# Kernel tuning notes

Measured on AMD Instinct MI355X. Metric: run time of the kernel, lower is better.

The kernel has to match this reference:

```python
import jax, jax.numpy as jnp
import numpy as np

N, E = 50000, 640000
FEAT, EMB, HID, B = 128, 128, 512, 32


def setup_inputs() -> dict:
    key = jax.random.key(0)
    ks = jax.random.split(key, 12)
    def w(k, shape, fan_in):
        return jax.random.normal(k, shape, dtype=jnp.float32) / np.sqrt(fan_in)
    return {
        "x": jax.random.normal(ks[0], (N, FEAT), dtype=jnp.float32),
        "edge_index": jax.random.randint(ks[1], (2, E), 0, N, dtype=jnp.int64),
        "last_hidden": jax.random.normal(ks[2], (1, B, HID), dtype=jnp.float32),
        "W1_rel": w(ks[3], (FEAT, EMB), FEAT),
        "W1_root": w(ks[4], (FEAT, EMB), FEAT),
        "b1": jnp.zeros((EMB,), dtype=jnp.float32),
        "W2_rel": w(ks[5], (EMB, EMB), EMB),
        "W2_root": w(ks[6], (EMB, EMB), EMB),
        "b2": jnp.zeros((EMB,), dtype=jnp.float32),
        "Wp": w(ks[7], (HID, EMB), HID),
        "bp": jnp.zeros((EMB,), dtype=jnp.float32),
    }


def _rgcn(h, src, dst, W_rel, W_root, b):
    # transform-then-gather (N < E so cheaper): messages along edges src->dst
    msg = (h @ W_rel)[src]                                   # [E, emb]
    agg = jax.ops.segment_sum(msg, dst, num_segments=N)      # [N, emb]
    deg = jax.ops.segment_sum(jnp.ones((E,), h.dtype), dst, num_segments=N)
    agg = agg / jnp.maximum(deg, 1.0)[:, None]               # mean aggregation (PyG RGCNConv default)
    return agg + h @ W_root + b


def reference(x, edge_index, last_hidden, W1_rel, W1_root, b1, W2_rel, W2_root, b2, Wp, bp):
    src, dst = edge_index[0], edge_index[1]
    h = jax.nn.relu(_rgcn(x, src, dst, W1_rel, W1_root, b1))   # [N, emb]
    h = jax.nn.relu(_rgcn(h, src, dst, W2_rel, W2_root, b2))   # [N, emb]
    message_embed = (last_hidden @ Wp + bp)[0]                 # squeeze(0) -> [B, emb]
    scores = h @ message_embed.T                               # [N, B]
    return jax.nn.log_softmax(scores, axis=0)
```

## Files before the change

kernel.cpp:

```cpp
#include <hip/hip_runtime.h>
#include <hip/hip_bf16.h>

#define N_NODES 50000
#define N_EDGES 640000
#define DUMMY   N_NODES
#define PAD_SSRC 990000

typedef __attribute__((ext_vector_type(8))) short short8;
typedef __attribute__((ext_vector_type(4))) float floatx4;

__device__ __forceinline__ float bf2f(unsigned short u) {
    return __uint_as_float(((unsigned int)u) << 16);
}
__device__ __forceinline__ unsigned short f2bf(float x) {
    unsigned int u = __float_as_uint(x);
    u = (u + 0x7fffu + ((u >> 16) & 1u)) >> 16;
    return (unsigned short)u;
}
__device__ __forceinline__ unsigned char f2f8(float x) {
    int pk = __builtin_amdgcn_cvt_pk_fp8_f32(x, x, 0, false);
    return (unsigned char)(pk & 0xff);
}

__global__ void __launch_bounds__(256) prep_k(const float* __restrict__ W0,
                                              const float* __restrict__ W1,
                                              const float* __restrict__ W2,
                                              const float* __restrict__ W3,
                                              unsigned short* __restrict__ T0,
                                              unsigned short* __restrict__ T1,
                                              unsigned short* __restrict__ T2,
                                              unsigned short* __restrict__ T3,
                                              int* __restrict__ cnt,
                                              const float* __restrict__ lh,
                                              const float* __restrict__ Wp,
                                              const float* __restrict__ bp,
                                              unsigned short* __restrict__ meb,
                                              unsigned short* __restrict__ ssrc,
                                              unsigned char* __restrict__ tbf,
                                              int* __restrict__ total,
                                              const int* __restrict__ dst,
                                              int* __restrict__ rank) {
    int b = blockIdx.x, tid = threadIdx.x;
    bool is_hist;
    int idx;
    if (b < 4414) { is_hist = ((b & 1) == 0); idx = b >> 1; }
    else          { is_hist = true;            idx = 2207 + (b - 4414); }
    if (is_hist) {
        int e = idx * 256 + tid;
        int d = dst[e];
        int r = atomicAdd(&cnt[d], 1);
        rank[e] = (r << 16) | d;
        return;
    }
    int s = idx;
    if (s < 256) {
        int i2 = s * 256 + tid;
        int w = i2 >> 14;
        int r = i2 & 16383;
        int n = r >> 7, k = r & 127;
        const float* W = (w == 0) ? W0 : (w == 1) ? W1 : (w == 2) ? W2 : W3;
        unsigned short* T = (w == 0) ? T0 : (w == 1) ? T1 : (w == 2) ? T2 : T3;
        T[r] = f2bf(W[k * 128 + n]);
    } else if (s < 272) {
        int o = (s - 256) * 256 + tid;
        int i = o >> 7, c = o & 127;
        float acc = bp[c];
        const float4* lr = (const float4*)(lh + i * 512);
        #pragma unroll 4
        for (int k4 = 0; k4 < 128; k4++) {
            float4 v = lr[k4];
            acc += v.x * Wp[(4 * k4 + 0) * 128 + c] + v.y * Wp[(4 * k4 + 1) * 128 + c]
                 + v.z * Wp[(4 * k4 + 2) * 128 + c] + v.w * Wp[(4 * k4 + 3) * 128 + c];
        }
        meb[o] = f2bf(acc);
    } else if (s < 2206) {
        int i = (s - 272) * 256 + tid;
        if (i < PAD_SSRC / 2) ((unsigned int*)ssrc)[i] = 0xC350C350u;
    } else {
        if (tid < 32) ((unsigned int*)(tbf + (size_t)DUMMY * 128))[tid] = 0;
        else if (tid == 32) *total = 0;
    }
}

template <bool AF32>
__device__ __forceinline__ void gemm_dual_body(int bid, int tid,
                                               const void* __restrict__ Ain,
                                               const unsigned short* __restrict__ BtRel,
                                               const unsigned short* __restrict__ BtRoot,
                                               unsigned char* __restrict__ Trel,
                                               unsigned short* __restrict__ Rootb, int M) {
    int wid = tid >> 6, lane = tid & 63;
    int r0 = bid * 32 + (wid >> 1) * 16;
    int ch = (wid & 1) * 64;
    int m = lane & 15, g = lane >> 4;
    int row = r0 + m;
    int rowc = (row < M) ? row : (M - 1);
    short8 a[4];
    if constexpr (AF32) {
        const float* A = (const float*)Ain;
        #pragma unroll
        for (int kt = 0; kt < 4; kt++) {
            const float* p = A + (size_t)rowc * 128 + kt * 32 + g * 8;
            float4 v0 = *(const float4*)p;
            float4 v1 = *(const float4*)(p + 4);
            short8 t;
            t[0] = (short)f2bf(v0.x); t[1] = (short)f2bf(v0.y);
            t[2] = (short)f2bf(v0.z); t[3] = (short)f2bf(v0.w);
            t[4] = (short)f2bf(v1.x); t[5] = (short)f2bf(v1.y);
            t[6] = (short)f2bf(v1.z); t[7] = (short)f2bf(v1.w);
            a[kt] = t;
        }
    } else {
        const unsigned short* A = (const unsigned short*)Ain;
        #pragma unroll
        for (int kt = 0; kt < 4; kt++)
            a[kt] = *(const short8*)(A + (size_t)rowc * 128 + kt * 32 + g * 8);
    }
    floatx4 accR[4], accO[4];
    #pragma unroll
    for (int ct = 0; ct < 4; ct++) {
        accR[ct] = (floatx4)(0.f);
        accO[ct] = (floatx4)(0.f);
    }
    #pragma unroll
    for (int ct = 0; ct < 4; ct++) {
        const unsigned short* br = BtRel  + (size_t)(ch + ct * 16 + m) * 128 + g * 8;
        const unsigned short* bo = BtRoot + (size_t)(ch + ct * 16 + m) * 128 + g * 8;
        short8 bR[4], bO[4];
        #pragma unroll
        for (int kt = 0; kt < 4; kt++) {
            bR[kt] = *(const short8*)(br + kt * 32);
            bO[kt] = *(const short8*)(bo + kt * 32);
        }
        #pragma unroll
        for (int kt = 0; kt < 4; kt++) {
            accR[ct] = __builtin_amdgcn_mfma_f32_16x16x32_bf16(a[kt], bR[kt], accR[ct], 0, 0, 0);
            accO[ct] = __builtin_amdgcn_mfma_f32_16x16x32_bf16(a[kt], bO[kt], accO[ct], 0, 0, 0);
        }
    }
    #pragma unroll
    for (int ct = 0; ct < 4; ct++) {
        #pragma unroll
        for (int rg = 0; rg < 4; rg++) {
            int ro = r0 + g * 4 + rg;
            if (ro < M) {
                int co = ch + ct * 16 + m;
                Trel[(size_t)ro * 128 + co]  = f2f8(accR[ct][rg]);
                Rootb[(size_t)ro * 128 + co] = f2bf(accO[ct][rg]);
            }
        }
    }
}

__global__ void __launch_bounds__(256) allocgemm_k(const int* __restrict__ cnt,
                                                   int* __restrict__ prow,
                                                   int* __restrict__ total,
                                                   const float* __restrict__ A,
                                                   const unsigned short* __restrict__ BtRel,
                                                   const unsigned short* __restrict__ BtRoot,
                                                   unsigned char* __restrict__ Trel,
                                                   unsigned short* __restrict__ Rootb) {
    if (blockIdx.x < 196) {
        __shared__ int sm[256];
        __shared__ int base_s;
        int t = threadIdx.x;
        int i = blockIdx.x * 256 + t;
        int pc = (i < N_NODES) ? ((cnt[i] + 7) & ~7) : 0;
        sm[t] = pc;
        __syncthreads();
        for (int off = 1; off < 256; off <<= 1) {
            int v = (t >= off) ? sm[t - off] : 0;
            __syncthreads();
            sm[t] += v;
            __syncthreads();
        }
        if (t == 255) base_s = atomicAdd(total, sm[255]);
        __syncthreads();
        if (i < N_NODES) prow[i] = base_s + sm[t] - pc;
    } else {
        gemm_dual_body<true>(blockIdx.x - 196, threadIdx.x, A, BtRel, BtRoot, Trel, Rootb, N_NODES);
    }
}

__global__ void __launch_bounds__(256) place_k(const int* __restrict__ src,
                                               const int* __restrict__ prow,
                                               const int* __restrict__ rank,
                                               unsigned short* __restrict__ ssrc) {
    int e = blockIdx.x * 256 + threadIdx.x;
    if (e < N_EDGES) {
        int pk = rank[e];
        int d = pk & 0xffff;
        int r = pk >> 16;
        ssrc[prow[d] + r] = (unsigned short)src[e];
    }
}

__global__ void __launch_bounds__(256) gemm_dual_k(const unsigned short* __restrict__ A,
                                                   const unsigned short* __restrict__ BtRel,
                                                   const unsigned short* __restrict__ BtRoot,
                                                   unsigned char* __restrict__ Trel,
                                                   unsigned short* __restrict__ Rootb, int M) {
    gemm_dual_body<false>(blockIdx.x, threadIdx.x, A, BtRel, BtRoot, Trel, Rootb, M);
}

__global__ void __launch_bounds__(256) agg_k(const int* __restrict__ prow,
                                             const int* __restrict__ cnt,
                                             const unsigned short* __restrict__ ssrc,
                                             const unsigned char* __restrict__ t,
                                             const unsigned short* __restrict__ rootb,
                                             const float* __restrict__ bias,
                                             unsigned short* __restrict__ hout) {
    int node = blockIdx.x * 4 + (threadIdx.x >> 6);
    if (node >= N_NODES) return;
    int lane = threadIdx.x & 63;
    int fl = lane & 31;
    int sh = (lane & 32) >> 1;
    int beg = prow[node];
    int deg = cnt[node];
    int endp = beg + ((deg + 7) & ~7);
    const unsigned char* tf = t + fl * 4;
    float a0=0.f,a1=0.f,a2=0.f,a3=0.f;
    float b0=0.f,b1=0.f,b2=0.f,b3=0.f;
    for (int e = beg; e < endp; e += 16) {
        uint4 w0 = *(const uint4*)(ssrc + e);
        uint4 w1 = (e + 8 < endp) ? *(const uint4*)(ssrc + e + 8)
                                  : make_uint4(0xC350C350u, 0xC350C350u, 0xC350C350u, 0xC350C350u);
        int i0 = (int)((w0.x >> sh) & 0xffffu);
        int i1 = (int)((w0.y >> sh) & 0xffffu);
        int i2 = (int)((w0.z >> sh) & 0xffffu);
        int i3 = (int)((w0.w >> sh) & 0xffffu);
        int i4 = (int)((w1.x >> sh) & 0xffffu);
        int i5 = (int)((w1.y >> sh) & 0xffffu);
        int i6 = (int)((w1.z >> sh) & 0xffffu);
        int i7 = (int)((w1.w >> sh) & 0xffffu);
        unsigned int u0 = *(const unsigned int*)(tf + (size_t)i0 * 128);
        unsigned int u1 = *(const unsigned int*)(tf + (size_t)i1 * 128);
        unsigned int u2 = *(const unsigned int*)(tf + (size_t)i2 * 128);
        unsigned int u3 = *(const unsigned int*)(tf + (size_t)i3 * 128);
        unsigned int u4 = *(const unsigned int*)(tf + (size_t)i4 * 128);
        unsigned int u5 = *(const unsigned int*)(tf + (size_t)i5 * 128);
        unsigned int u6 = *(const unsigned int*)(tf + (size_t)i6 * 128);
        unsigned int u7 = *(const unsigned int*)(tf + (size_t)i7 * 128);
        a0 += __builtin_amdgcn_cvt_f32_fp8(u0, 0) + __builtin_amdgcn_cvt_f32_fp8(u1, 0);
        a1 += __builtin_amdgcn_cvt_f32_fp8(u0, 1) + __builtin_amdgcn_cvt_f32_fp8(u1, 1);
        a2 += __builtin_amdgcn_cvt_f32_fp8(u0, 2) + __builtin_amdgcn_cvt_f32_fp8(u1, 2);
        a3 += __builtin_amdgcn_cvt_f32_fp8(u0, 3) + __builtin_amdgcn_cvt_f32_fp8(u1, 3);
        b0 += __builtin_amdgcn_cvt_f32_fp8(u2, 0) + __builtin_amdgcn_cvt_f32_fp8(u3, 0);
        b1 += __builtin_amdgcn_cvt_f32_fp8(u2, 1) + __builtin_amdgcn_cvt_f32_fp8(u3, 1);
        b2 += __builtin_amdgcn_cvt_f32_fp8(u2, 2) + __builtin_amdgcn_cvt_f32_fp8(u3, 2);
        b3 += __builtin_amdgcn_cvt_f32_fp8(u2, 3) + __builtin_amdgcn_cvt_f32_fp8(u3, 3);
        a0 += __builtin_amdgcn_cvt_f32_fp8(u4, 0) + __builtin_amdgcn_cvt_f32_fp8(u5, 0);
        a1 += __builtin_amdgcn_cvt_f32_fp8(u4, 1) + __builtin_amdgcn_cvt_f32_fp8(u5, 1);
        a2 += __builtin_amdgcn_cvt_f32_fp8(u4, 2) + __builtin_amdgcn_cvt_f32_fp8(u5, 2);
        a3 += __builtin_amdgcn_cvt_f32_fp8(u4, 3) + __builtin_amdgcn_cvt_f32_fp8(u5, 3);
        b0 += __builtin_amdgcn_cvt_f32_fp8(u6, 0) + __builtin_amdgcn_cvt_f32_fp8(u7, 0);
        b1 += __builtin_amdgcn_cvt_f32_fp8(u6, 1) + __builtin_amdgcn_cvt_f32_fp8(u7, 1);
        b2 += __builtin_amdgcn_cvt_f32_fp8(u6, 2) + __builtin_amdgcn_cvt_f32_fp8(u7, 2);
        b3 += __builtin_amdgcn_cvt_f32_fp8(u6, 3) + __builtin_amdgcn_cvt_f32_fp8(u7, 3);
    }
    a0 += b0; a1 += b1; a2 += b2; a3 += b3;
    a0 += __shfl_xor(a0, 32);
    a1 += __shfl_xor(a1, 32);
    a2 += __shfl_xor(a2, 32);
    a3 += __shfl_xor(a3, 32);
    if ((lane & 32) == 0) {
        float inv = 1.f / fmaxf((float)deg, 1.f);
        int f = fl * 4;
        ushort4 r = *(const ushort4*)(rootb + (size_t)node * 128 + f);
        float4 bb = *(const float4*)(bias + f);
        ushort4 o;
        o.x = f2bf(fmaxf(a0 * inv + bf2f(r.x) + bb.x, 0.f));
        o.y = f2bf(fmaxf(a1 * inv + bf2f(r.y) + bb.y, 0.f));
        o.z = f2bf(fmaxf(a2 * inv + bf2f(r.z) + bb.z, 0.f));
        o.w = f2bf(fmaxf(a3 * inv + bf2f(r.w) + bb.w, 0.f));
        *(ushort4*)(hout + (size_t)node * 128 + f) = o;
    }
}

__global__ void __launch_bounds__(256) scores_cs_k(const unsigned short* __restrict__ A,
                                                   const unsigned short* __restrict__ Bt,
                                                   float* __restrict__ S,
                                                   float* __restrict__ pm,
                                                   float* __restrict__ ps) {
    __shared__ float Sl[64][33];
    __shared__ float sm[256], ss[256];
    int tid = threadIdx.x;
    int wid = tid >> 6, lane = tid & 63;
    int r0 = blockIdx.x * 64 + wid * 16;
    int m = lane & 15, g = lane >> 4;
    int row = r0 + m;
    int rowc = (row < N_NODES) ? row : (N_NODES - 1);
    short8 a[4];
    #pragma unroll
    for (int kt = 0; kt < 4; kt++)
        a[kt] = *(const short8*)(A + (size_t)rowc * 128 + kt * 32 + g * 8);
    floatx4 acc[2];
    acc[0] = (floatx4)(0.f);
    acc[1] = (floatx4)(0.f);
    #pragma unroll
    for (int ct = 0; ct < 2; ct++) {
        const unsigned short* b = Bt + (size_t)(ct * 16 + m) * 128 + g * 8;
        #pragma unroll
        for (int kt = 0; kt < 4; kt++) {
            short8 bv = *(const short8*)(b + kt * 32);
            acc[ct] = __builtin_amdgcn_mfma_f32_16x16x32_bf16(a[kt], bv, acc[ct], 0, 0, 0);
        }
    }
    #pragma unroll
    for (int ct = 0; ct < 2; ct++) {
        #pragma unroll
        for (int rg = 0; rg < 4; rg++) {
            int lr = wid * 16 + g * 4 + rg;
            int ro = r0 + g * 4 + rg;
            Sl[lr][ct * 16 + m] = acc[ct][rg];
            if (ro < N_NODES) S[(size_t)ro * 32 + ct * 16 + m] = acc[ct][rg];
        }
    }
    __syncthreads();
    int col = tid & 31, sub = tid >> 5;
    int blkbase = blockIdx.x * 64;
    float mm = -3.4e38f, s = 0.f;
    for (int r = sub; r < 64; r += 8) {
        if (blkbase + r < N_NODES) {
            float v = Sl[r][col];
            if (v > mm) { s = s * __expf(mm - v) + 1.f; mm = v; }
            else        { s += __expf(v - mm); }
        }
    }
    sm[tid] = mm; ss[tid] = s;
    __syncthreads();
    for (int off = 128; off >= 32; off >>= 1) {
        if (tid < off) {
            float m2 = sm[tid + off], s2 = ss[tid + off];
            float M = fmaxf(sm[tid], m2);
            ss[tid] = ss[tid] * __expf(sm[tid] - M) + s2 * __expf(m2 - M);
            sm[tid] = M;
        }
        __syncthreads();
    }
    if (tid < 32) { pm[tid * 782 + blockIdx.x] = sm[tid]; ps[tid * 782 + blockIdx.x] = ss[tid]; }
}

__global__ void __launch_bounds__(256) merge_k(const float* __restrict__ pm,
                                               const float* __restrict__ ps,
                                               float* __restrict__ cmg,
                                               float* __restrict__ clg) {
    __shared__ float sm[256], ss[256];
    int col = blockIdx.x;
    int t = threadIdx.x;
    float m = -3.4e38f, s = 0.f;
    for (int c = t; c < 782; c += 256) {
        float m2 = pm[col * 782 + c], s2 = ps[col * 782 + c];
        float M = fmaxf(m, m2);
        s = s * __expf(m - M) + s2 * __expf(m2 - M);
        m = M;
    }
    sm[t] = m; ss[t] = s;
    __syncthreads();
    for (int off = 128; off > 0; off >>= 1) {
        if (t < off) {
            float m2 = sm[t + off], s2 = ss[t + off];
            float M = fmaxf(sm[t], m2);
            ss[t] = ss[t] * __expf(sm[t] - M) + s2 * __expf(m2 - M);
            sm[t] = M;
        }
        __syncthreads();
    }
    if (t == 0) { cmg[col] = sm[0]; clg[col] = logf(ss[0]); }
}

__global__ void __launch_bounds__(256) final_k(const float* __restrict__ S,
                                               const float* __restrict__ cmg,
                                               const float* __restrict__ clg,
                                               float* __restrict__ out) {
    __shared__ float cc[32];
    int t = threadIdx.x;
    if (t < 32) cc[t] = cmg[t] + clg[t];
    __syncthreads();
    int idx = blockIdx.x * 256 + t;
    if (idx < N_NODES * 32) {
        int b = idx & 31;
        out[idx] = S[idx] - cc[b];
    }
}

extern "C" void kernel_launch(void* const* d_in, const int* in_sizes, int n_in,
                              void* d_out, int out_size, void* d_ws, size_t ws_size,
                              hipStream_t stream) {
    const float* x       = (const float*)d_in[0];
    const int*   ei      = (const int*)d_in[1];
    const float* lh      = (const float*)d_in[2];
    const float* W1_rel  = (const float*)d_in[3];
    const float* W1_root = (const float*)d_in[4];
    const float* b1      = (const float*)d_in[5];
    const float* W2_rel  = (const float*)d_in[6];
    const float* W2_root = (const float*)d_in[7];
    const float* b2      = (const float*)d_in[8];
    const float* Wp      = (const float*)d_in[9];
    const float* bp      = (const float*)d_in[10];
    float* out = (float*)d_out;
    float* ws  = (float*)d_ws;

    unsigned char*  tbf   = (unsigned char*)(ws + 3200000);
    unsigned short* rootb = (unsigned short*)(ws + 4800032);
    unsigned short* hb    = (unsigned short*)(ws + 8000032);
    unsigned short* Wt1r  = (unsigned short*)(ws + 11200032);
    unsigned short* Wt1o  = (unsigned short*)(ws + 11208224);
    unsigned short* Wt2r  = (unsigned short*)(ws + 11216416);
    unsigned short* Wt2o  = (unsigned short*)(ws + 11224608);
    unsigned short* MEb   = (unsigned short*)(ws + 11232800);
    float* pm   = ws + 11234848;
    float* ps   = ws + 11259872;
    float* cmg  = ws + 11284896;
    float* clg  = ws + 11284928;
    int*   cnt  = (int*)(ws + 11284960);
    int*   prow = (int*)(ws + 11334960);
    int*   total= (int*)(ws + 11384961);
    int*   rank = (int*)(ws + 11384964);
    unsigned short* ssrc = (unsigned short*)(ws + 12024964);
    float* S    = ws + 12519964;

    const int* srcp = ei;
    const int* dstp = ei + N_EDGES;

    const int e_grid   = (N_EDGES + 255) / 256;
    const int ew_grid  = (N_NODES * 32 + 255) / 256;
    const int agg_grid = (N_NODES + 3) / 4;
    const int mm_grid  = (N_NODES + 63) / 64;
    const int g32_grid = (N_NODES + 31) / 32;

    hipMemsetAsync(cnt, 0, N_NODES * sizeof(int), stream);

    prep_k<<<4707, 256, 0, stream>>>(W1_rel, W1_root, W2_rel, W2_root,
                                     Wt1r, Wt1o, Wt2r, Wt2o,
                                     cnt, lh, Wp, bp, MEb, ssrc, tbf, total,
                                     dstp, rank);

    allocgemm_k<<<196 + g32_grid, 256, 0, stream>>>(cnt, prow, total,
                                                    x, Wt1r, Wt1o, tbf, rootb);

    place_k<<<e_grid, 256, 0, stream>>>(srcp, prow, rank, ssrc);

    agg_k<<<agg_grid, 256, 0, stream>>>(prow, cnt, ssrc, tbf, rootb, b1, hb);

    gemm_dual_k<<<g32_grid, 256, 0, stream>>>(hb, Wt2r, Wt2o, tbf, rootb, N_NODES);

    agg_k<<<agg_grid, 256, 0, stream>>>(prow, cnt, ssrc, tbf, rootb, b2, hb);

    scores_cs_k<<<mm_grid, 256, 0, stream>>>(hb, MEb, S, pm, ps);

    merge_k<<<32, 256, 0, stream>>>(pm, ps, cmg, clg);

    final_k<<<ew_grid, 256, 0, stream>>>(S, cmg, clg, out);
}
```

Baseline: 259.2 us.

## Privatize degree histogram per XCC to avoid cross-die atomics

```diff
diff --git a/kernel.cpp b/kernel.cpp
--- a/kernel.cpp
+++ b/kernel.cpp
@@ -30,7 +30,7 @@
                                               unsigned short* __restrict__ T1,
                                               unsigned short* __restrict__ T2,
                                               unsigned short* __restrict__ T3,
-                                              int* __restrict__ cnt,
+                                              int* __restrict__ cnt8,
                                               const float* __restrict__ lh,
                                               const float* __restrict__ Wp,
                                               const float* __restrict__ bp,
@@ -48,8 +48,12 @@
     if (is_hist) {
         int e = idx * 256 + tid;
         int d = dst[e];
-        int r = atomicAdd(&cnt[d], 1);
-        rank[e] = (r << 16) | d;
+        int xcc;
+        asm volatile("s_getreg_b32 %0, hwreg(HW_REG_XCC_ID)" : "=s"(xcc));
+        xcc &= 7;
+        int r = __hip_atomic_fetch_add(&cnt8[xcc * N_NODES + d], 1,
+                                       __ATOMIC_RELAXED, __HIP_MEMORY_SCOPE_WORKGROUP);
+        rank[e] = (r << 19) | (xcc << 16) | d;
         return;
     }
     int s = idx;
@@ -152,8 +156,10 @@
     }
 }
 
-__global__ void __launch_bounds__(256) allocgemm_k(const int* __restrict__ cnt,
+__global__ void __launch_bounds__(256) allocgemm_k(const int* __restrict__ cnt8,
+                                                   int* __restrict__ cnt,
                                                    int* __restrict__ prow,
+                                                   int* __restrict__ poff,
                                                    int* __restrict__ total,
                                                    const float* __restrict__ A,
                                                    const unsigned short* __restrict__ BtRel,
@@ -165,7 +171,13 @@
         __shared__ int base_s;
         int t = threadIdx.x;
         int i = blockIdx.x * 256 + t;
-        int pc = (i < N_NODES) ? ((cnt[i] + 7) & ~7) : 0;
+        int deg = 0;
+        int pre[8];
+        if (i < N_NODES) {
+            #pragma unroll
+            for (int c = 0; c < 8; c++) { pre[c] = deg; deg += cnt8[c * N_NODES + i]; }
+        }
+        int pc = (i < N_NODES) ? ((deg + 7) & ~7) : 0;
         sm[t] = pc;
         __syncthreads();
         for (int off = 1; off < 256; off <<= 1) {
@@ -176,22 +188,29 @@
         }
         if (t == 255) base_s = atomicAdd(total, sm[255]);
         __syncthreads();
-        if (i < N_NODES) prow[i] = base_s + sm[t] - pc;
+        if (i < N_NODES) {
+            int base = base_s + sm[t] - pc;
+            prow[i] = base;
+            cnt[i] = deg;
+            #pragma unroll
+            for (int c = 0; c < 8; c++) poff[i * 8 + c] = base + pre[c];
+        }
     } else {
         gemm_dual_body<true>(blockIdx.x - 196, threadIdx.x, A, BtRel, BtRoot, Trel, Rootb, N_NODES);
     }
 }
 
 __global__ void __launch_bounds__(256) place_k(const int* __restrict__ src,
-                                               const int* __restrict__ prow,
+                                               const int* __restrict__ poff,
                                                const int* __restrict__ rank,
                                                unsigned short* __restrict__ ssrc) {
     int e = blockIdx.x * 256 + threadIdx.x;
     if (e < N_EDGES) {
         int pk = rank[e];
         int d = pk & 0xffff;
-        int r = pk >> 16;
-        ssrc[prow[d] + r] = (unsigned short)src[e];
+        int c = (pk >> 16) & 7;
+        int r = (int)(((unsigned)pk) >> 19);
+        ssrc[poff[d * 8 + c] + r] = (unsigned short)src[e];
     }
 }
 
@@ -419,6 +438,8 @@
     int*   rank = (int*)(ws + 11384964);
     unsigned short* ssrc = (unsigned short*)(ws + 12024964);
     float* S    = ws + 12519964;
+    int*   cnt8 = (int*)(ws + 12519964);
+    int*   poff = (int*)(ws + 12519964 + 400000);
 
     const int* srcp = ei;
     const int* dstp = ei + N_EDGES;
@@ -429,17 +450,17 @@
     const int mm_grid  = (N_NODES + 63) / 64;
     const int g32_grid = (N_NODES + 31) / 32;
 
-    hipMemsetAsync(cnt, 0, N_NODES * sizeof(int), stream);
+    hipMemsetAsync(cnt8, 0, 8 * N_NODES * sizeof(int), stream);
 
     prep_k<<<4707, 256, 0, stream>>>(W1_rel, W1_root, W2_rel, W2_root,
                                      Wt1r, Wt1o, Wt2r, Wt2o,
-                                     cnt, lh, Wp, bp, MEb, ssrc, tbf, total,
+                                     cnt8, lh, Wp, bp, MEb, ssrc, tbf, total,
                                      dstp, rank);
 
-    allocgemm_k<<<196 + g32_grid, 256, 0, stream>>>(cnt, prow, total,
+    allocgemm_k<<<196 + g32_grid, 256, 0, stream>>>(cnt8, cnt, prow, poff, total,
                                                     x, Wt1r, Wt1o, tbf, rootb);
 
-    place_k<<<e_grid, 256, 0, stream>>>(srcp, prow, rank, ssrc);
+    place_k<<<e_grid, 256, 0, stream>>>(srcp, poff, rank, ssrc);
 
     agg_k<<<agg_grid, 256, 0, stream>>>(prow, cnt, ssrc, tbf, rootb, b1, hb);
 
```

Measured after the change: 259.7 us. No clear change (+0.2%).

## Fuse neighbor aggregation with following GEMM and scores via LDS-staged tiles

Applied to the files above, without the earlier changes.

```diff
diff --git a/kernel.cpp b/kernel.cpp
--- a/kernel.cpp
+++ b/kernel.cpp
@@ -37,6 +37,7 @@
                                               unsigned short* __restrict__ meb,
                                               unsigned short* __restrict__ ssrc,
                                               unsigned char* __restrict__ tbf,
+                                              unsigned char* __restrict__ tbf2,
                                               int* __restrict__ total,
                                               const int* __restrict__ dst,
                                               int* __restrict__ rank) {
@@ -77,45 +78,21 @@
         int i = (s - 272) * 256 + tid;
         if (i < PAD_SSRC / 2) ((unsigned int*)ssrc)[i] = 0xC350C350u;
     } else {
-        if (tid < 32) ((unsigned int*)(tbf + (size_t)DUMMY * 128))[tid] = 0;
-        else if (tid == 32) *total = 0;
-    }
-}
-
-template <bool AF32>
-__device__ __forceinline__ void gemm_dual_body(int bid, int tid,
-                                               const void* __restrict__ Ain,
-                                               const unsigned short* __restrict__ BtRel,
-                                               const unsigned short* __restrict__ BtRoot,
-                                               unsigned char* __restrict__ Trel,
-                                               unsigned short* __restrict__ Rootb, int M) {
+        if (tid < 32)       ((unsigned int*)(tbf  + (size_t)DUMMY * 128))[tid] = 0;
+        else if (tid < 64)  ((unsigned int*)(tbf2 + (size_t)DUMMY * 128))[tid - 32] = 0;
+        else if (tid == 64) *total = 0;
+    }
+}
+
+__device__ __forceinline__ void gemm_dual_frags(int bid, int tid, const short8 a[4],
+                                                const unsigned short* __restrict__ BtRel,
+                                                const unsigned short* __restrict__ BtRoot,
+                                                unsigned char* __restrict__ Trel,
+                                                unsigned short* __restrict__ Rootb, int M) {
     int wid = tid >> 6, lane = tid & 63;
     int r0 = bid * 32 + (wid >> 1) * 16;
     int ch = (wid & 1) * 64;
     int m = lane & 15, g = lane >> 4;
-    int row = r0 + m;
-    int rowc = (row < M) ? row : (M - 1);
-    short8 a[4];
-    if constexpr (AF32) {
-        const float* A = (const float*)Ain;
-        #pragma unroll
-        for (int kt = 0; kt < 4; kt++) {
-            const float* p = A + (size_t)rowc * 128 + kt * 32 + g * 8;
-            float4 v0 = *(const float4*)p;
-            float4 v1 = *(const float4*)(p + 4);
-            short8 t;
-            t[0] = (short)f2bf(v0.x); t[1] = (short)f2bf(v0.y);
-            t[2] = (short)f2bf(v0.z); t[3] = (short)f2bf(v0.w);
-            t[4] = (short)f2bf(v1.x); t[5] = (short)f2bf(v1.y);
-            t[6] = (short)f2bf(v1.z); t[7] = (short)f2bf(v1.w);
-            a[kt] = t;
-        }
-    } else {
-        const unsigned short* A = (const unsigned short*)Ain;
-        #pragma unroll
-        for (int kt = 0; kt < 4; kt++)
-            a[kt] = *(const short8*)(A + (size_t)rowc * 128 + kt * 32 + g * 8);
-    }
     floatx4 accR[4], accO[4];
     #pragma unroll
     for (int ct = 0; ct < 4; ct++) {
@@ -178,7 +155,26 @@
         __syncthreads();
         if (i < N_NODES) prow[i] = base_s + sm[t] - pc;
     } else {
-        gemm_dual_body<true>(blockIdx.x - 196, threadIdx.x, A, BtRel, BtRoot, Trel, Rootb, N_NODES);
+        int bid = blockIdx.x - 196, tid = threadIdx.x;
+        int wid = tid >> 6, lane = tid & 63;
+        int r0 = bid * 32 + (wid >> 1) * 16;
+        int m = lane & 15, g = lane >> 4;
+        int row = r0 + m;
+        int rowc = (row < N_NODES) ? row : (N_NODES - 1);
+        short8 a[4];
+        #pragma unroll
+        for (int kt = 0; kt < 4; kt++) {
+            const float* p = A + (size_t)rowc * 128 + kt * 32 + g * 8;
+            float4 v0 = *(const float4*)p;
+            float4 v1 = *(const float4*)(p + 4);
+            short8 t8;
+            t8[0] = (short)f2bf(v0.x); t8[1] = (short)f2bf(v0.y);
+            t8[2] = (short)f2bf(v0.z); t8[3] = (short)f2bf(v0.w);
+            t8[4] = (short)f2bf(v1.x); t8[5] = (short)f2bf(v1.y);
+            t8[6] = (short)f2bf(v1.z); t8[7] = (short)f2bf(v1.w);
+            a[kt] = t8;
+        }
+        gemm_dual_frags(bid, tid, a, BtRel, BtRoot, Trel, Rootb, N_NODES);
     }
 }
 
@@ -195,105 +191,166 @@
     }
 }
 
-__global__ void __launch_bounds__(256) gemm_dual_k(const unsigned short* __restrict__ A,
-                                                   const unsigned short* __restrict__ BtRel,
-                                                   const unsigned short* __restrict__ BtRoot,
-                                                   unsigned char* __restrict__ Trel,
-                                                   unsigned short* __restrict__ Rootb, int M) {
-    gemm_dual_body<false>(blockIdx.x, threadIdx.x, A, BtRel, BtRoot, Trel, Rootb, M);
-}
-
-__global__ void __launch_bounds__(256) agg_k(const int* __restrict__ prow,
-                                             const int* __restrict__ cnt,
-                                             const unsigned short* __restrict__ ssrc,
-                                             const unsigned char* __restrict__ t,
-                                             const unsigned short* __restrict__ rootb,
-                                             const float* __restrict__ bias,
-                                             unsigned short* __restrict__ hout) {
-    int node = blockIdx.x * 4 + (threadIdx.x >> 6);
-    if (node >= N_NODES) return;
-    int lane = threadIdx.x & 63;
-    int fl = lane & 31;
-    int sh = (lane & 32) >> 1;
-    int beg = prow[node];
-    int deg = cnt[node];
-    int endp = beg + ((deg + 7) & ~7);
-    const unsigned char* tf = t + fl * 4;
+__device__ __forceinline__ void agg_gather(int node, int sh,
+                                           const int* __restrict__ prow,
+                                           const int* __restrict__ cnt,
+                                           const unsigned short* __restrict__ ssrc,
+                                           const unsigned char* __restrict__ tf,
+                                           float& A0, float& A1, float& A2, float& A3,
+                                           int& DEG) {
     float a0=0.f,a1=0.f,a2=0.f,a3=0.f;
     float b0=0.f,b1=0.f,b2=0.f,b3=0.f;
-    for (int e = beg; e < endp; e += 16) {
-        uint4 w0 = *(const uint4*)(ssrc + e);
-        uint4 w1 = (e + 8 < endp) ? *(const uint4*)(ssrc + e + 8)
-                                  : make_uint4(0xC350C350u, 0xC350C350u, 0xC350C350u, 0xC350C350u);
-        int i0 = (int)((w0.x >> sh) & 0xffffu);
-        int i1 = (int)((w0.y >> sh) & 0xffffu);
-        int i2 = (int)((w0.z >> sh) & 0xffffu);
-        int i3 = (int)((w0.w >> sh) & 0xffffu);
-        int i4 = (int)((w1.x >> sh) & 0xffffu);
-        int i5 = (int)((w1.y >> sh) & 0xffffu);
-        int i6 = (int)((w1.z >> sh) & 0xffffu);
-        int i7 = (int)((w1.w >> sh) & 0xffffu);
-        unsigned int u0 = *(const unsigned int*)(tf + (size_t)i0 * 128);
-        unsigned int u1 = *(const unsigned int*)(tf + (size_t)i1 * 128);
-        unsigned int u2 = *(const unsigned int*)(tf + (size_t)i2 * 128);
-        unsigned int u3 = *(const unsigned int*)(tf + (size_t)i3 * 128);
-        unsigned int u4 = *(const unsigned int*)(tf + (size_t)i4 * 128);
-        unsigned int u5 = *(const unsigned int*)(tf + (size_t)i5 * 128);
-        unsigned int u6 = *(const unsigned int*)(tf + (size_t)i6 * 128);
-        unsigned int u7 = *(const unsigned int*)(tf + (size_t)i7 * 128);
-        a0 += __builtin_amdgcn_cvt_f32_fp8(u0, 0) + __builtin_amdgcn_cvt_f32_fp8(u1, 0);
-        a1 += __builtin_amdgcn_cvt_f32_fp8(u0, 1) + __builtin_amdgcn_cvt_f32_fp8(u1, 1);
-        a2 += __builtin_amdgcn_cvt_f32_fp8(u0, 2) + __builtin_amdgcn_cvt_f32_fp8(u1, 2);
-        a3 += __builtin_amdgcn_cvt_f32_fp8(u0, 3) + __builtin_amdgcn_cvt_f32_fp8(u1, 3);
-        b0 += __builtin_amdgcn_cvt_f32_fp8(u2, 0) + __builtin_amdgcn_cvt_f32_fp8(u3, 0);
-        b1 += __builtin_amdgcn_cvt_f32_fp8(u2, 1) + __builtin_amdgcn_cvt_f32_fp8(u3, 1);
-        b2 += __builtin_amdgcn_cvt_f32_fp8(u2, 2) + __builtin_amdgcn_cvt_f32_fp8(u3, 2);
-        b3 += __builtin_amdgcn_cvt_f32_fp8(u2, 3) + __builtin_amdgcn_cvt_f32_fp8(u3, 3);
-        a0 += __builtin_amdgcn_cvt_f32_fp8(u4, 0) + __builtin_amdgcn_cvt_f32_fp8(u5, 0);
-        a1 += __builtin_amdgcn_cvt_f32_fp8(u4, 1) + __builtin_amdgcn_cvt_f32_fp8(u5, 1);
-        a2 += __builtin_amdgcn_cvt_f32_fp8(u4, 2) + __builtin_amdgcn_cvt_f32_fp8(u5, 2);
-        a3 += __builtin_amdgcn_cvt_f32_fp8(u4, 3) + __builtin_amdgcn_cvt_f32_fp8(u5, 3);
-        b0 += __builtin_amdgcn_cvt_f32_fp8(u6, 0) + __builtin_amdgcn_cvt_f32_fp8(u7, 0);
-        b1 += __builtin_amdgcn_cvt_f32_fp8(u6, 1) + __builtin_amdgcn_cvt_f32_fp8(u7, 1);
-        b2 += __builtin_amdgcn_cvt_f32_fp8(u6, 2) + __builtin_amdgcn_cvt_f32_fp8(u7, 2);
-        b3 += __builtin_amdgcn_cvt_f32_fp8(u6, 3) + __builtin_amdgcn_cvt_f32_fp8(u7, 3);
+    int deg = 0;
+    if (node < N_NODES) {
+        int beg = prow[node];
+        deg = cnt[node];
+        int endp = beg + ((deg + 7) & ~7);
+        for (int e = beg; e < endp; e += 16) {
+            uint4 w0 = *(const uint4*)(ssrc + e);
+            uint4 w1 = (e + 8 < endp) ? *(const uint4*)(ssrc + e + 8)
+                                      : make_uint4(0xC350C350u, 0xC350C350u, 0xC350C350u, 0xC350C350u);
+            int i0 = (int)((w0.x >> sh) & 0xffffu);
+            int i1 = (int)((w0.y >> sh) & 0xffffu);
+            int i2 = (int)((w0.z >> sh) & 0xffffu);
+            int i3 = (int)((w0.w >> sh) & 0xffffu);
+            int i4 = (int)((w1.x >> sh) & 0xffffu);
+            int i5 = (int)((w1.y >> sh) & 0xffffu);
+            int i6 = (int)((w1.z >> sh) & 0xffffu);
+            int i7 = (int)((w1.w >> sh) & 0xffffu);
+            unsigned int u0 = *(const unsigned int*)(tf + (size_t)i0 * 128);
+            unsigned int u1 = *(const unsigned int*)(tf + (size_t)i1 * 128);
+            unsigned int u2 = *(const unsigned int*)(tf + (size_t)i2 * 128);
+            unsigned int u3 = *(const unsigned int*)(tf + (size_t)i3 * 128);
+            unsigned int u4 = *(const unsigned int*)(tf + (size_t)i4 * 128);
+            unsigned int u5 = *(const unsigned int*)(tf + (size_t)i5 * 128);
+            unsigned int u6 = *(const unsigned int*)(tf + (size_t)i6 * 128);
+            unsigned int u7 = *(const unsigned int*)(tf + (size_t)i7 * 128);
+            a0 += __builtin_amdgcn_cvt_f32_fp8(u0, 0) + __builtin_amdgcn_cvt_f32_fp8(u1, 0);
+            a1 += __builtin_amdgcn_cvt_f32_fp8(u0, 1) + __builtin_amdgcn_cvt_f32_fp8(u1, 1);
+            a2 += __builtin_amdgcn_cvt_f32_fp8(u0, 2) + __builtin_amdgcn_cvt_f32_fp8(u1, 2);
+            a3 += __builtin_amdgcn_cvt_f32_fp8(u0, 3) + __builtin_amdgcn_cvt_f32_fp8(u1, 3);
+            b0 += __builtin_amdgcn_cvt_f32_fp8(u2, 0) + __builtin_amdgcn_cvt_f32_fp8(u3, 0);
+            b1 += __builtin_amdgcn_cvt_f32_fp8(u2, 1) + __builtin_amdgcn_cvt_f32_fp8(u3, 1);
+            b2 += __builtin_amdgcn_cvt_f32_fp8(u2, 2) + __builtin_amdgcn_cvt_f32_fp8(u3, 2);
+            b3 += __builtin_amdgcn_cvt_f32_fp8(u2, 3) + __builtin_amdgcn_cvt_f32_fp8(u3, 3);
+            a0 += __builtin_amdgcn_cvt_f32_fp8(u4, 0) + __builtin_amdgcn_cvt_f32_fp8(u5, 0);
+            a1 += __builtin_amdgcn_cvt_f32_fp8(u4, 1) + __builtin_amdgcn_cvt_f32_fp8(u5, 1);
+            a2 += __builtin_amdgcn_cvt_f32_fp8(u4, 2) + __builtin_amdgcn_cvt_f32_fp8(u5, 2);
+            a3 += __builtin_amdgcn_cvt_f32_fp8(u4, 3) + __builtin_amdgcn_cvt_f32_fp8(u5, 3);
+            b0 += __builtin_amdgcn_cvt_f32_fp8(u6, 0) + __builtin_amdgcn_cvt_f32_fp8(u7, 0);
+            b1 += __builtin_amdgcn_cvt_f32_fp8(u6, 1) + __builtin_amdgcn_cvt_f32_fp8(u7, 1);
+            b2 += __builtin_amdgcn_cvt_f32_fp8(u6, 2) + __builtin_amdgcn_cvt_f32_fp8(u7, 2);
+            b3 += __builtin_amdgcn_cvt_f32_fp8(u6, 3) + __builtin_amdgcn_cvt_f32_fp8(u7, 3);
+        }
     }
     a0 += b0; a1 += b1; a2 += b2; a3 += b3;
     a0 += __shfl_xor(a0, 32);
     a1 += __shfl_xor(a1, 32);
     a2 += __shfl_xor(a2, 32);
     a3 += __shfl_xor(a3, 32);
-    if ((lane & 32) == 0) {
-        float inv = 1.f / fmaxf((float)deg, 1.f);
-        int f = fl * 4;
-        ushort4 r = *(const ushort4*)(rootb + (size_t)node * 128 + f);
-        float4 bb = *(const float4*)(bias + f);
-        ushort4 o;
-        o.x = f2bf(fmaxf(a0 * inv + bf2f(r.x) + bb.x, 0.f));
-        o.y = f2bf(fmaxf(a1 * inv + bf2f(r.y) + bb.y, 0.f));
-        o.z = f2bf(fmaxf(a2 * inv + bf2f(r.z) + bb.z, 0.f));
-        o.w = f2bf(fmaxf(a3 * inv + bf2f(r.w) + bb.w, 0.f));
-        *(ushort4*)(hout + (size_t)node * 128 + f) = o;
-    }
-}
-
-__global__ void __launch_bounds__(256) scores_cs_k(const unsigned short* __restrict__ A,
+    A0 = a0; A1 = a1; A2 = a2; A3 = a3; DEG = deg;
+}
+
+__global__ void __launch_bounds__(256) aggemm_k(const int* __restrict__ prow,
+                                                const int* __restrict__ cnt,
+                                                const unsigned short* __restrict__ ssrc,
+                                                const unsigned char* __restrict__ t,
+                                                const unsigned short* __restrict__ rootb,
+                                                const float* __restrict__ bias,
+                                                const unsigned short* __restrict__ BtRel,
+                                                const unsigned short* __restrict__ BtRoot,
+                                                unsigned char* __restrict__ Trel2,
+                                                unsigned short* __restrict__ Rootb2) {
+    __shared__ __align__(16) unsigned short hl[32 * 128];
+    int tid = threadIdx.x;
+    int lane = tid & 63;
+    int fl = lane & 31;
+    int sh = (lane & 32) >> 1;
+    const unsigned char* tf = t + fl * 4;
+    for (int r8 = 0; r8 < 8; r8++) {
+        int nl = r8 * 4 + (tid >> 6);
+        int node = blockIdx.x * 32 + nl;
+        float a0, a1, a2, a3; int deg;
+        agg_gather(node, sh, prow, cnt, ssrc, tf, a0, a1, a2, a3, deg);
+        if ((lane & 32) == 0) {
+            int f = fl * 4;
+            ushort4 o;
+            if (node < N_NODES) {
+                float inv = 1.f / fmaxf((float)deg, 1.f);
+                ushort4 r = *(const ushort4*)(rootb + (size_t)node * 128 + f);
+                float4 bb = *(const float4*)(bias + f);
+                o.x = f2bf(fmaxf(a0 * inv + bf2f(r.x) + bb.x, 0.f));
+                o.y = f2bf(fmaxf(a1 * inv + bf2f(r.y) + bb.y, 0.f));
+                o.z = f2bf(fmaxf(a2 * inv + bf2f(r.z) + bb.z, 0.f));
+                o.w = f2bf(fmaxf(a3 * inv + bf2f(r.w) + bb.w, 0.f));
+            } else { o.x = o.y = o.z = o.w = 0; }
+            int byte = (nl * 256 + f * 2) ^ ((nl & 7) << 4);
+            *(ushort4*)((char*)hl + byte) = o;
+        }
+    }
+    __syncthreads();
+    int wid = tid >> 6;
+    int m = lane & 15, g = lane >> 4;
+    int lr = (wid >> 1) * 16 + m;
+    short8 a[4];
+    #pragma unroll
+    for (int kt = 0; kt < 4; kt++) {
+        int byte = (lr * 256 + kt * 64 + g * 16) ^ ((lr & 7) << 4);
+        a[kt] = *(const short8*)((const char*)hl + byte);
+    }
+    gemm_dual_frags(blockIdx.x, tid, a, BtRel, BtRoot, Trel2, Rootb2, N_NODES);
+}
+
+__global__ void __launch_bounds__(256) aggscores_k(const int* __restrict__ prow,
+                                                   const int* __restrict__ cnt,
+                                                   const unsigned short* __restrict__ ssrc,
+                                                   const unsigned char* __restrict__ t,
+                                                   const unsigned short* __restrict__ rootb2,
+                                                   const float* __restrict__ bias,
                                                    const unsigned short* __restrict__ Bt,
                                                    float* __restrict__ S,
                                                    float* __restrict__ pm,
                                                    float* __restrict__ ps) {
+    __shared__ __align__(16) unsigned short hl[64 * 128];
     __shared__ float Sl[64][33];
     __shared__ float sm[256], ss[256];
     int tid = threadIdx.x;
-    int wid = tid >> 6, lane = tid & 63;
+    int lane = tid & 63;
+    int fl = lane & 31;
+    int sh = (lane & 32) >> 1;
+    const unsigned char* tf = t + fl * 4;
+    for (int r16 = 0; r16 < 16; r16++) {
+        int nl = r16 * 4 + (tid >> 6);
+        int node = blockIdx.x * 64 + nl;
+        float a0, a1, a2, a3; int deg;
+        agg_gather(node, sh, prow, cnt, ssrc, tf, a0, a1, a2, a3, deg);
+        if ((lane & 32) == 0) {
+            int f = fl * 4;
+            ushort4 o;
+            if (node < N_NODES) {
+                float inv = 1.f / fmaxf((float)deg, 1.f);
+                ushort4 r = *(const ushort4*)(rootb2 + (size_t)node * 128 + f);
+                float4 bb = *(const float4*)(bias + f);
+                o.x = f2bf(fmaxf(a0 * inv + bf2f(r.x) + bb.x, 0.f));
+                o.y = f2bf(fmaxf(a1 * inv + bf2f(r.y) + bb.y, 0.f));
+                o.z = f2bf(fmaxf(a2 * inv + bf2f(r.z) + bb.z, 0.f));
+                o.w = f2bf(fmaxf(a3 * inv + bf2f(r.w) + bb.w, 0.f));
+            } else { o.x = o.y = o.z = o.w = 0; }
+            int byte = (nl * 256 + f * 2) ^ ((nl & 7) << 4);
+            *(ushort4*)((char*)hl + byte) = o;
+        }
+    }
+    __syncthreads();
+    int wid = tid >> 6;
     int r0 = blockIdx.x * 64 + wid * 16;
     int m = lane & 15, g = lane >> 4;
-    int row = r0 + m;
-    int rowc = (row < N_NODES) ? row : (N_NODES - 1);
+    int lrA = wid * 16 + m;
     short8 a[4];
     #pragma unroll
-    for (int kt = 0; kt < 4; kt++)
-        a[kt] = *(const short8*)(A + (size_t)rowc * 128 + kt * 32 + g * 8);
+    for (int kt = 0; kt < 4; kt++) {
+        int byte = (lrA * 256 + kt * 64 + g * 16) ^ ((lrA & 7) << 4);
+        a[kt] = *(const short8*)((const char*)hl + byte);
+    }
     floatx4 acc[2];
     acc[0] = (floatx4)(0.f);
     acc[1] = (floatx4)(0.f);
@@ -401,9 +458,10 @@
     float* out = (float*)d_out;
     float* ws  = (float*)d_ws;
 
+    unsigned short* rootb2= (unsigned short*)(ws);
     unsigned char*  tbf   = (unsigned char*)(ws + 3200000);
     unsigned short* rootb = (unsigned short*)(ws + 4800032);
-    unsigned short* hb    = (unsigned short*)(ws + 8000032);
+    unsigned char*  tbf2  = (unsigned char*)(ws + 8000032);
     unsigned short* Wt1r  = (unsigned short*)(ws + 11200032);
     unsigned short* Wt1o  = (unsigned short*)(ws + 11208224);
     unsigned short* Wt2r  = (unsigned short*)(ws + 11216416);
@@ -425,7 +483,6 @@
 
     const int e_grid   = (N_EDGES + 255) / 256;
     const int ew_grid  = (N_NODES * 32 + 255) / 256;
-    const int agg_grid = (N_NODES + 3) / 4;
     const int mm_grid  = (N_NODES + 63) / 64;
     const int g32_grid = (N_NODES + 31) / 32;
 
@@ -433,7 +490,7 @@
 
     prep_k<<<4707, 256, 0, stream>>>(W1_rel, W1_root, W2_rel, W2_root,
                                      Wt1r, Wt1o, Wt2r, Wt2o,
-                                     cnt, lh, Wp, bp, MEb, ssrc, tbf, total,
+                                     cnt, lh, Wp, bp, MEb, ssrc, tbf, tbf2, total,
                                      dstp, rank);
 
     allocgemm_k<<<196 + g32_grid, 256, 0, stream>>>(cnt, prow, total,
@@ -441,13 +498,11 @@
 
     place_k<<<e_grid, 256, 0, stream>>>(srcp, prow, rank, ssrc);
 
-    agg_k<<<agg_grid, 256, 0, stream>>>(prow, cnt, ssrc, tbf, rootb, b1, hb);
-
-    gemm_dual_k<<<g32_grid, 256, 0, stream>>>(hb, Wt2r, Wt2o, tbf, rootb, N_NODES);
-
-    agg_k<<<agg_grid, 256, 0, stream>>>(prow, cnt, ssrc, tbf, rootb, b2, hb);
-
-    scores_cs_k<<<mm_grid, 256, 0, stream>>>(hb, MEb, S, pm, ps);
+    aggemm_k<<<g32_grid, 256, 0, stream>>>(prow, cnt, ssrc, tbf, rootb, b1,
+                                           Wt2r, Wt2o, tbf2, rootb2);
+
+    aggscores_k<<<mm_grid, 256, 0, stream>>>(prow, cnt, ssrc, tbf2, rootb2, b2,
+                                             MEb, S, pm, ps);
 
     merge_k<<<32, 256, 0, stream>>>(pm, ps, cmg, clg);
 
```

New measurement: 270.2 us. 4.2% more time.
